# Optimization experiments

Hardware: AMD Instinct MI355X
Metric: run time of the kernel (lower is better)

Reference implementation:

```python
import jax, jax.numpy as jnp
from jax import lax
import numpy as np

NBC, NAC, KF, RHO = 14, 45, 52, 0.05
KT = np.arange(0.8, 0, -1.0 / 64, dtype=np.float32)[None, :]  # (1, 52) AC kernel time axis
K = KT.shape[1]


def _sigm(x, off, slope):
    return jax.nn.sigmoid(slope * (x - off))


def _ac_kernel(log_tr, log_td, kt):
    tr = jnp.exp(log_tr)[:, None]  # (nAC,1)
    td = jnp.exp(log_td)[:, None]
    k = jnp.exp(-kt / td) - jnp.exp(-(td + tr) / (td * tr) * kt)  # (nAC,K)
    return k / jnp.linalg.norm(k, axis=1, keepdims=True)


def setup_inputs() -> dict:
    key = jax.random.key(0)
    ks = jax.random.split(key, 12)
    B, T = 64, 4096
    n = 0.01  # noise_init_scale
    return {
        "x": jax.random.normal(ks[0], (B, T), jnp.float32) * 0.5,
        "bc_kernels": jax.random.normal(ks[1], (NBC, KF), jnp.float32) * 0.1,
        "log_sigmoid_slope": jnp.log(2.0) + n * jax.random.normal(ks[2], (NBC,), jnp.float32),
        "sigmoid_offset": 1.5 + n * jax.random.normal(ks[3], (NBC,), jnp.float32),
        "log_bc_ac_weight": jnp.log(1.0 / NBC) + n * jax.random.normal(ks[4], (NAC, NBC), jnp.float32),
        "log_ac_tau_rise": jnp.log(0.1) + n * jax.random.normal(ks[5], (NAC,), jnp.float32),
        "log_ac_tau_decay": jnp.log(0.1) + n * jax.random.normal(ks[6], (NAC,), jnp.float32),
        "log_ac_sigmoid_slope": jnp.log(2.0) + n * jax.random.normal(ks[7], (NAC,), jnp.float32),
        "ac_sigmoid_offset": 1.5 + n * jax.random.normal(ks[8], (NAC,), jnp.float32),
        "log_ac_bc_weight": jnp.log(0.01) + n * jax.random.normal(ks[9], (NBC, NAC), jnp.float32),
        "out_scale": jnp.ones((NBC,), jnp.float32),
    }


def reference(x, bc_kernels, log_sigmoid_slope, sigmoid_offset, log_bc_ac_weight,
              log_ac_tau_rise, log_ac_tau_decay, log_ac_sigmoid_slope,
              ac_sigmoid_offset, log_ac_bc_weight, out_scale):
    B, T = x.shape
    kt = jnp.asarray(KT)
    # linear_filter: causal conv of stimulus with per-BC kernels -> (T, B, nBC)
    xf = lax.conv_general_dilated(x[:, None, :], bc_kernels[:, None, :], (1,), [(KF - 1, 0)])
    xf = jnp.transpose(xf, (2, 0, 1))  # (T, B, nBC)

    slope = jnp.exp(log_sigmoid_slope)
    ac_slope = jnp.exp(log_ac_sigmoid_slope)
    bc_ac_w = jnp.exp(log_bc_ac_weight)          # (nAC, nBC)
    ac_bc_w = -jnp.exp(log_ac_bc_weight)         # (nBC, nAC)
    ack = _ac_kernel(log_ac_tau_rise, log_ac_tau_decay, kt)  # (nAC, K)

    # --- plain LNR branch (no feedback) ---
    prob_lnr = _sigm(xf, sigmoid_offset, slope)

    def lnr_step(pool, p):
        pool2 = pool + (1.0 - pool) * RHO
        rel = p * pool2
        return pool2 - rel, rel

    _, rel_lnr = lax.scan(lnr_step, jnp.ones((B, NBC), x.dtype), prob_lnr)
    y_lnr = (out_scale * rel_lnr).transpose(1, 0, 2)  # (B, T, nBC)

    # --- BCN branch with AC feedback recurrence ---
    def bcn_step(carry, xt):
        pool, prev_rel, buf = carry
        # append previous release (track_release[i-1]) to sliding window (oldest first)
        buf = jnp.concatenate([buf[..., 1:], prev_rel[..., None]], axis=-1)  # (B, nBC, K)
        drive = jnp.einsum('ak,ab,nbk->na', ack, bc_ac_w, buf)               # (B, nAC)
        ac_out = _sigm(drive, ac_sigmoid_offset, ac_slope)
        fb = ac_out @ ac_bc_w.T                                              # (B, nBC)
        prob = _sigm(xt + fb, sigmoid_offset, slope)
        pool2 = pool + (1.0 - pool) * RHO
        rel = prob * pool2
        return (pool2 - rel, rel, buf), (rel, fb, ac_out)

    init = (jnp.ones((B, NBC), x.dtype), jnp.zeros((B, NBC), x.dtype), jnp.zeros((B, NBC, K), x.dtype))
    _, (rel, fb, ac_out) = lax.scan(bcn_step, init, xf)
    y_bcn = (out_scale * rel).transpose(1, 0, 2)  # (B, T, nBC)
    return y_bcn, fb.transpose(1, 0, 2), ac_out.transpose(1, 0, 2), y_lnr
```

## Files before the change

### kernel.cpp

```cpp
#include <hip/hip_runtime.h>
#include <hip/hip_fp16.h>

#define NBC 14
#define NAC 45
#define KF  52
#define RHO 0.05f
#define TT  4096
#define BB  64
#define CHC 64
#define WU  44
#define NPAIR 32
#define NTW (WU + CHC)
#define SPAN (WU + 2*CHC)
#define XPAD 176
#define LOG2E 1.44269504f
#define XF_BYTES ((size_t)BB * NBC * TT * 2)

typedef __fp16 v2h __attribute__((ext_vector_type(2)));
typedef float  f2  __attribute__((ext_vector_type(2)));
typedef int    i2v __attribute__((ext_vector_type(2)));

__device__ __forceinline__ v2h bch(unsigned u) { return __builtin_bit_cast(v2h, u); }
__device__ __forceinline__ unsigned bcu(v2h h) { return __builtin_bit_cast(unsigned, h); }
__device__ __forceinline__ v2h pk2(float lo, float hi) {
#if __has_builtin(__builtin_amdgcn_cvt_pkrtz)
  return __builtin_bit_cast(v2h, __builtin_amdgcn_cvt_pkrtz(lo, hi));
#else
  v2h r; r[0] = (__fp16)lo; r[1] = (__fp16)hi; return r;
#endif
}
__device__ __forceinline__ v2h xsum16h(v2h v) {
#if __has_builtin(__builtin_amdgcn_permlane16_swap)
  i2v r = __builtin_amdgcn_permlane16_swap((int)bcu(v), (int)bcu(v), false, false);
  return bch((unsigned)r[0]) + bch((unsigned)r[1]);
#else
  return v + bch((unsigned)__builtin_amdgcn_ds_swizzle((int)bcu(v), (16 << 10) | 0x1f));
#endif
}
__device__ __forceinline__ v2h xsum32h(v2h v) {
#if __has_builtin(__builtin_amdgcn_permlane32_swap)
  i2v r = __builtin_amdgcn_permlane32_swap((int)bcu(v), (int)bcu(v), false, false);
  return bch((unsigned)r[0]) + bch((unsigned)r[1]);
#else
  return v + bch((unsigned)__shfl_xor((int)bcu(v), 32));
#endif
}
__device__ __forceinline__ float exp2_f(float x) {
#if __has_builtin(__builtin_amdgcn_exp2f)
  return __builtin_amdgcn_exp2f(x);
#else
  return exp2f(x);
#endif
}

__global__ __launch_bounds__(256)
void conv_kernel(const float* __restrict__ x, const float* __restrict__ bck,
                 __half* __restrict__ xfg) {
  __shared__ float xs[256 + KF];
  const int tid  = threadIdx.x;
  const int b    = blockIdx.x >> 4;
  const int t0   = (blockIdx.x & 15) << 8;
  for (int i = tid; i < 256 + KF - 1; i += 256) {
    int gt = t0 - (KF - 1) + i;
    xs[i] = (gt >= 0) ? x[b * TT + gt] : 0.f;
  }
  __syncthreads();
  float acc[NBC];
#pragma unroll
  for (int c = 0; c < NBC; ++c) acc[c] = 0.f;
#pragma unroll 4
  for (int k = 0; k < KF; ++k) {
    float xv = xs[tid + k];
#pragma unroll
    for (int c = 0; c < NBC; ++c) acc[c] = fmaf(bck[c * KF + k], xv, acc[c]);
  }
#pragma unroll
  for (int c = 0; c < NBC; ++c)
    xfg[((size_t)b * NBC + c) * TT + t0 + tid] = __float2half(acc[c]);
}

#define POOL_BYTES 6144

template<bool PRECONV>
__global__ __launch_bounds__(64)
void bcn_kernel(const float* __restrict__ x,
                const float* __restrict__ bck,
                const float* __restrict__ lss,
                const float* __restrict__ soff,
                const float* __restrict__ lbaw,
                const float* __restrict__ ltr,
                const float* __restrict__ ltd,
                const float* __restrict__ lass,
                const float* __restrict__ asoff,
                const float* __restrict__ labw,
                const float* __restrict__ oscale,
                const __half* __restrict__ xfg,
                float* __restrict__ out)
{
  __shared__ __align__(16) char pool[POOL_BYTES];
  __half*   xf_lds = (__half*)pool;
  unsigned* acr    = (unsigned*)(pool + 4928);
  unsigned* relr   = (unsigned*)(pool + 5184);
  float*    x_lds  = (float*)(pool + 5248);

  const int lid   = threadIdx.x;
  const int c16   = lid & 15;
  const int q     = lid >> 4;
  const float rowm = (q & 1) ? 0.f : 1.f;
  const int blk   = blockIdx.x;
  const int b     = blk >> 5;
  const int p     = blk & 31;
  const int t0A   = p * (2 * CHC);
  const int t_begin = t0A - WU;

  if constexpr (PRECONV) {
    const __half* src = xfg + (size_t)b * NBC * TT;
    if (p == 0) {
      for (int e = lid; e < NBC * SPAN; e += 64) {
        int c = e / SPAN, i = e - c * SPAN;
        int gt = t_begin + i; if (gt < 0) gt = 0;
        xf_lds[c * XPAD + i] = src[(size_t)c * TT + gt];
      }
    } else {
      for (int c = 0; c < NBC; ++c) {
        if (lid < SPAN / 4) {
          uint2 v = *(const uint2*)(src + (size_t)c * TT + t_begin + 4 * lid);
          *(uint2*)&xf_lds[c * XPAD + 4 * lid] = v;
        }
      }
    }
  } else {
    for (int i = lid; i < SPAN + KF - 1; i += 64) {
      int gt = t_begin - (KF - 1) + i;
      x_lds[i] = (gt >= 0) ? x[b * TT + gt] : 0.f;
    }
    __syncthreads();
    for (int ib = 0; ib < 3; ++ib) {
      int tau = lid + (ib << 6);
      if (tau < SPAN) {
        float acc[NBC];
#pragma unroll
        for (int c = 0; c < NBC; ++c) acc[c] = 0.f;
#pragma unroll 4
        for (int k = 0; k < KF; ++k) {
          float xv = x_lds[tau + k];
#pragma unroll
          for (int c = 0; c < NBC; ++c) acc[c] = fmaf(bck[c * KF + k], xv, acc[c]);
        }
#pragma unroll
        for (int c = 0; c < NBC; ++c) xf_lds[c * XPAD + tau] = __float2half(acc[c]);
      }
    }
    __syncthreads();
  }

  if (lid < 64) acr[lid] = 0u;
  if (lid < 16) relr[lid] = 0u;

  float slope2 = 0.f, soff2 = 0.f, osc_c = 0.f;
  f2 poolP; poolP.x = 1.f; poolP.y = 1.f;
  f2 SA; SA.x = 0.f; SA.y = 0.f;
  f2 SB; SB.x = 0.f; SB.y = 0.f;
  f2 rv2, cn2; rv2.x = rv2.y = cn2.x = cn2.y = 0.f;
  float Adrv2 = 0.f, Boff2 = 0.f;
  v2h wfbh[16];
  v2h wuh[NBC];
  f2 yst[4], fst[4];
  unsigned acst[4];

#pragma unroll
  for (int j = 0; j < 16; ++j) wfbh[j] = pk2(0.f, 0.f);
#pragma unroll
  for (int c = 0; c < NBC; ++c) wuh[c] = pk2(0.f, 0.f);

  if (c16 < NBC) {
    float sl = expf(lss[c16]);
    slope2 = sl * LOG2E;
    soff2  = soff[c16] * sl * LOG2E;
    osc_c  = oscale[c16];
#pragma unroll
    for (int j = 0; j < 16; ++j) {
      int a = 16 * q + j;
      if (a < NAC) { float w = -expf(labw[c16 * NAC + a]); wfbh[j] = pk2(w, w); }
    }
  }
  if (lid < NAC) {
    float tr = expf(ltr[lid]);
    float td = expf(ltd[lid]);
    float a1 = 1.f / td;
    float gg = (td + tr) / (td * tr);
    rv2.x = expf(-a1 * 0.015625f);  rv2.y = expf(-gg * 0.015625f);
    cn2.x = expf(-a1 * 0.003125f);  cn2.y = expf(-gg * 0.003125f);
    float nrm = 0.f;
    for (int k = 0; k < KF; ++k) {
      float kt = 0.8f - (float)k * 0.015625f;
      float d = expf(-a1 * kt) - expf(-gg * kt);
      nrm = fmaf(d, d, nrm);
    }
    float inorm  = 1.f / sqrtf(nrm);
    float aslope = expf(lass[lid]);
    Adrv2 = aslope * inorm * LOG2E;
    Boff2 = aslope * asoff[lid] * LOG2E;
#pragma unroll
    for (int c = 0; c < NBC; ++c) {
      float w = expf(lbaw[lid * NBC + c]);
      wuh[c] = pk2(w, w);
    }
  }

  float* yb  = out;
  float* fbp = out + (size_t)BB * TT * NBC;
  float* acp = out + 2 * (size_t)BB * TT * NBC;
  float* ylp = out + 2 * (size_t)BB * TT * NBC + (size_t)BB * TT * NAC;

  __syncthreads();

  auto step = [&](int slot4, float xfA, float xfB, bool emit)
      __attribute__((always_inline)) {
    float mzA = fmaf(-Adrv2, SA.x - SA.y, Boff2);
    float mzB = fmaf(-Adrv2, SB.x - SB.y, Boff2);
    float acA = __fdividef(1.f, 1.f + exp2_f(mzA));
    float acB = __fdividef(1.f, 1.f + exp2_f(mzB));
    if (lid < NAC) acr[lid] = bcu(pk2(acA, acB));

    const uint4* ab = (const uint4*)(acr + (q << 4));
    uint4 A0 = ab[0], A1 = ab[1], A2 = ab[2], A3 = ab[3];
    v2h g0 = wfbh[0] * bch(A0.x);
    v2h g1 = wfbh[1] * bch(A0.y);
    g0 += wfbh[2]  * bch(A0.z);  g1 += wfbh[3]  * bch(A0.w);
    g0 += wfbh[4]  * bch(A1.x);  g1 += wfbh[5]  * bch(A1.y);
    g0 += wfbh[6]  * bch(A1.z);  g1 += wfbh[7]  * bch(A1.w);
    g0 += wfbh[8]  * bch(A2.x);  g1 += wfbh[9]  * bch(A2.y);
    g0 += wfbh[10] * bch(A2.z);  g1 += wfbh[11] * bch(A2.w);
    g0 += wfbh[12] * bch(A3.x);  g1 += wfbh[13] * bch(A3.y);
    g0 += wfbh[14] * bch(A3.z);  g1 += wfbh[15] * bch(A3.w);
    v2h gs = xsum32h(xsum16h(g0 + g1));
    float fbA = (float)gs[0], fbB = (float)gs[1];

    float mA = fmaf(-slope2, fmaf(rowm, fbA, xfA), soff2);
    float mB = fmaf(-slope2, fmaf(rowm, fbB, xfB), soff2);
    f2 pv;
    pv.x = __fdividef(1.f, 1.f + exp2_f(mA));
    pv.y = __fdividef(1.f, 1.f + exp2_f(mB));
    f2 p2 = poolP * (1.f - RHO) + RHO;
    f2 relP = pv * p2;
    poolP = p2 - relP;
    if (lid < NBC) relr[lid] = bcu(pk2(relP.x, relP.y));
    if (emit) {
      yst[slot4] = relP * osc_c;
      f2 t; t.x = fbA; t.y = fbB; fst[slot4] = t;
      acst[slot4] = bcu(pk2(acA, acB));
    }

    const uint4* rb = (const uint4*)relr;
    uint4 R0 = rb[0], R1 = rb[1], R2 = rb[2], R3 = rb[3];
    v2h h0 = wuh[0] * bch(R0.x);
    v2h h1 = wuh[1] * bch(R0.y);
    h0 += wuh[2]  * bch(R0.z);  h1 += wuh[3]  * bch(R0.w);
    h0 += wuh[4]  * bch(R1.x);  h1 += wuh[5]  * bch(R1.y);
    h0 += wuh[6]  * bch(R1.z);  h1 += wuh[7]  * bch(R1.w);
    h0 += wuh[8]  * bch(R2.x);  h1 += wuh[9]  * bch(R2.y);
    h0 += wuh[10] * bch(R2.z);  h1 += wuh[11] * bch(R2.w);
    h0 += wuh[12] * bch(R3.x);  h1 += wuh[13] * bch(R3.y);
    v2h uh = h0 + h1;
    SA = SA * rv2 + cn2 * (float)uh[0];
    SB = SB * rv2 + cn2 * (float)uh[1];
  };

  auto group = [&](int s4, bool emit) __attribute__((always_inline)) {
    uint2 xa = *(const uint2*)&xf_lds[c16 * XPAD + s4];
    uint2 xb = *(const uint2*)&xf_lds[c16 * XPAD + s4 + CHC];
    v2h xA01 = bch(xa.x), xA23 = bch(xa.y);
    v2h xB01 = bch(xb.x), xB23 = bch(xb.y);
    step(0, (float)xA01[0], (float)xB01[0], emit);
    step(1, (float)xA01[1], (float)xB01[1], emit);
    step(2, (float)xA23[0], (float)xB23[0], emit);
    step(3, (float)xA23[1], (float)xB23[1], emit);
  };

  for (int s4 = 0; s4 < WU; s4 += 4) group(s4, false);

  if (p == 0) {
    SA.x = 0.f; SA.y = 0.f;
    poolP.x = 1.f;
  }

  for (int s4 = WU; s4 < NTW; s4 += 4) {
    group(s4, true);

    int tgA = t0A + (s4 - WU);
    size_t baseA = (size_t)b * TT + tgA;
    if (lid < NBC) {
      size_t ob = baseA * NBC + lid;
#pragma unroll
      for (int sl = 0; sl < 4; ++sl) {
        yb [ob + sl * NBC]                     = yst[sl].x;
        yb [ob + (size_t)CHC * NBC + sl * NBC] = yst[sl].y;
        fbp[ob + sl * NBC]                     = fst[sl].x;
        fbp[ob + (size_t)CHC * NBC + sl * NBC] = fst[sl].y;
      }
    } else if (lid >= 16 && lid < 16 + NBC) {
      size_t ob = baseA * NBC + (lid - 16);
#pragma unroll
      for (int sl = 0; sl < 4; ++sl) {
        ylp[ob + sl * NBC]                     = yst[sl].x;
        ylp[ob + (size_t)CHC * NBC + sl * NBC] = yst[sl].y;
      }
    }
    if (lid < NAC) {
      size_t oa = baseA * NAC + lid;
#pragma unroll
      for (int sl = 0; sl < 4; ++sl) {
        v2h h = bch(acst[sl]);
        acp[oa + sl * NAC]                     = (float)h[0];
        acp[oa + (size_t)CHC * NAC + sl * NAC] = (float)h[1];
      }
    }
  }
}

extern "C" void kernel_launch(void* const* d_in, const int* in_sizes, int n_in,
                              void* d_out, int out_size, void* d_ws, size_t ws_size,
                              hipStream_t stream) {
  (void)in_sizes; (void)n_in; (void)out_size;
  const float* x    = (const float*)d_in[0];
  const float* bck  = (const float*)d_in[1];
  if (ws_size >= XF_BYTES) {
    __half* xfg = (__half*)d_ws;
    conv_kernel<<<dim3(BB * 16), dim3(256), 0, stream>>>(x, bck, xfg);
    bcn_kernel<true><<<dim3(BB * NPAIR), dim3(64), 0, stream>>>(
        x, bck, (const float*)d_in[2], (const float*)d_in[3], (const float*)d_in[4],
        (const float*)d_in[5], (const float*)d_in[6], (const float*)d_in[7],
        (const float*)d_in[8], (const float*)d_in[9], (const float*)d_in[10],
        xfg, (float*)d_out);
  } else {
    bcn_kernel<false><<<dim3(BB * NPAIR), dim3(64), 0, stream>>>(
        x, bck, (const float*)d_in[2], (const float*)d_in[3], (const float*)d_in[4],
        (const float*)d_in[5], (const float*)d_in[6], (const float*)d_in[7],
        (const float*)d_in[8], (const float*)d_in[9], (const float*)d_in[10],
        (const __half*)nullptr, (float*)d_out);
  }
}
```

Measured before the change: 91.35 us.

## Process four time chunks per wavefront instead of two in BCN recurrence

```diff
diff --git a/kernel.cpp b/kernel.cpp
--- a/kernel.cpp
+++ b/kernel.cpp
@@ -9,10 +9,10 @@
 #define BB  64
 #define CHC 64
 #define WU  44
-#define NPAIR 32
+#define NQUAD 16
 #define NTW (WU + CHC)
-#define SPAN (WU + 2*CHC)
-#define XPAD 176
+#define SPAN (WU + 4*CHC)
+#define XPAD 304
 #define LOG2E 1.44269504f
 #define XF_BYTES ((size_t)BB * NBC * TT * 2)
 
@@ -79,7 +79,7 @@
     xfg[((size_t)b * NBC + c) * TT + t0 + tid] = __float2half(acc[c]);
 }
 
-#define POOL_BYTES 6144
+#define POOL_BYTES 10560
 
 template<bool PRECONV>
 __global__ __launch_bounds__(64)
@@ -99,18 +99,20 @@
 {
   __shared__ __align__(16) char pool[POOL_BYTES];
   __half*   xf_lds = (__half*)pool;
-  unsigned* acr    = (unsigned*)(pool + 4928);
-  unsigned* relr   = (unsigned*)(pool + 5184);
-  float*    x_lds  = (float*)(pool + 5248);
+  unsigned* acr1   = (unsigned*)(pool + 8512);
+  unsigned* acr2   = (unsigned*)(pool + 8768);
+  unsigned* relr1  = (unsigned*)(pool + 9024);
+  unsigned* relr2  = (unsigned*)(pool + 9088);
+  float*    x_lds  = (float*)(pool + 9152);
 
   const int lid   = threadIdx.x;
   const int c16   = lid & 15;
   const int q     = lid >> 4;
   const float rowm = (q & 1) ? 0.f : 1.f;
   const int blk   = blockIdx.x;
-  const int b     = blk >> 5;
-  const int p     = blk & 31;
-  const int t0A   = p * (2 * CHC);
+  const int b     = blk >> 4;
+  const int p     = blk & 15;
+  const int t0A   = p * (4 * CHC);
   const int t_begin = t0A - WU;
 
   if constexpr (PRECONV) {
@@ -122,11 +124,10 @@
         xf_lds[c * XPAD + i] = src[(size_t)c * TT + gt];
       }
     } else {
-      for (int c = 0; c < NBC; ++c) {
-        if (lid < SPAN / 4) {
-          uint2 v = *(const uint2*)(src + (size_t)c * TT + t_begin + 4 * lid);
-          *(uint2*)&xf_lds[c * XPAD + 4 * lid] = v;
-        }
+      for (int e = lid; e < NBC * (SPAN / 4); e += 64) {
+        int c = e / (SPAN / 4), i = e - c * (SPAN / 4);
+        uint2 v = *(const uint2*)(src + (size_t)c * TT + t_begin + 4 * i);
+        *(uint2*)&xf_lds[c * XPAD + 4 * i] = v;
       }
     }
   } else {
@@ -135,7 +136,7 @@
       x_lds[i] = (gt >= 0) ? x[b * TT + gt] : 0.f;
     }
     __syncthreads();
-    for (int ib = 0; ib < 3; ++ib) {
+    for (int ib = 0; ib < 5; ++ib) {
       int tau = lid + (ib << 6);
       if (tau < SPAN) {
         float acc[NBC];
@@ -154,19 +155,22 @@
     __syncthreads();
   }
 
-  if (lid < 64) acr[lid] = 0u;
-  if (lid < 16) relr[lid] = 0u;
+  if (lid < 64) { acr1[lid] = 0u; acr2[lid] = 0u; }
+  if (lid < 16) { relr1[lid] = 0u; relr2[lid] = 0u; }
 
   float slope2 = 0.f, soff2 = 0.f, osc_c = 0.f;
-  f2 poolP; poolP.x = 1.f; poolP.y = 1.f;
+  f2 poolP1; poolP1.x = 1.f; poolP1.y = 1.f;
+  f2 poolP2; poolP2.x = 1.f; poolP2.y = 1.f;
   f2 SA; SA.x = 0.f; SA.y = 0.f;
   f2 SB; SB.x = 0.f; SB.y = 0.f;
+  f2 SC; SC.x = 0.f; SC.y = 0.f;
+  f2 SD; SD.x = 0.f; SD.y = 0.f;
   f2 rv2, cn2; rv2.x = rv2.y = cn2.x = cn2.y = 0.f;
   float Adrv2 = 0.f, Boff2 = 0.f;
   v2h wfbh[16];
   v2h wuh[NBC];
-  f2 yst[4], fst[4];
-  unsigned acst[4];
+  f2 yst1[4], fst1[4], yst2[4], fst2[4];
+  unsigned acst1[4], acst2[4];
 
 #pragma unroll
   for (int j = 0; j < 16; ++j) wfbh[j] = pk2(0.f, 0.f);
@@ -215,105 +219,151 @@
 
   __syncthreads();
 
-  auto step = [&](int slot4, float xfA, float xfB, bool emit)
+  auto step = [&](int slot4, float xA, float xB, float xC, float xD, bool emit)
       __attribute__((always_inline)) {
     float mzA = fmaf(-Adrv2, SA.x - SA.y, Boff2);
     float mzB = fmaf(-Adrv2, SB.x - SB.y, Boff2);
+    float mzC = fmaf(-Adrv2, SC.x - SC.y, Boff2);
+    float mzD = fmaf(-Adrv2, SD.x - SD.y, Boff2);
     float acA = __fdividef(1.f, 1.f + exp2_f(mzA));
     float acB = __fdividef(1.f, 1.f + exp2_f(mzB));
-    if (lid < NAC) acr[lid] = bcu(pk2(acA, acB));
-
-    const uint4* ab = (const uint4*)(acr + (q << 4));
-    uint4 A0 = ab[0], A1 = ab[1], A2 = ab[2], A3 = ab[3];
-    v2h g0 = wfbh[0] * bch(A0.x);
-    v2h g1 = wfbh[1] * bch(A0.y);
-    g0 += wfbh[2]  * bch(A0.z);  g1 += wfbh[3]  * bch(A0.w);
-    g0 += wfbh[4]  * bch(A1.x);  g1 += wfbh[5]  * bch(A1.y);
-    g0 += wfbh[6]  * bch(A1.z);  g1 += wfbh[7]  * bch(A1.w);
-    g0 += wfbh[8]  * bch(A2.x);  g1 += wfbh[9]  * bch(A2.y);
-    g0 += wfbh[10] * bch(A2.z);  g1 += wfbh[11] * bch(A2.w);
-    g0 += wfbh[12] * bch(A3.x);  g1 += wfbh[13] * bch(A3.y);
-    g0 += wfbh[14] * bch(A3.z);  g1 += wfbh[15] * bch(A3.w);
-    v2h gs = xsum32h(xsum16h(g0 + g1));
-    float fbA = (float)gs[0], fbB = (float)gs[1];
-
-    float mA = fmaf(-slope2, fmaf(rowm, fbA, xfA), soff2);
-    float mB = fmaf(-slope2, fmaf(rowm, fbB, xfB), soff2);
-    f2 pv;
-    pv.x = __fdividef(1.f, 1.f + exp2_f(mA));
-    pv.y = __fdividef(1.f, 1.f + exp2_f(mB));
-    f2 p2 = poolP * (1.f - RHO) + RHO;
-    f2 relP = pv * p2;
-    poolP = p2 - relP;
-    if (lid < NBC) relr[lid] = bcu(pk2(relP.x, relP.y));
+    float acC = __fdividef(1.f, 1.f + exp2_f(mzC));
+    float acD = __fdividef(1.f, 1.f + exp2_f(mzD));
+    if (lid < NAC) { acr1[lid] = bcu(pk2(acA, acB)); acr2[lid] = bcu(pk2(acC, acD)); }
+
+    const uint4* ab1 = (const uint4*)(acr1 + (q << 4));
+    const uint4* ab2 = (const uint4*)(acr2 + (q << 4));
+    uint4 P0 = ab1[0], P1 = ab1[1], P2 = ab1[2], P3 = ab1[3];
+    uint4 Q0 = ab2[0], Q1 = ab2[1], Q2 = ab2[2], Q3 = ab2[3];
+    v2h g0 = wfbh[0] * bch(P0.x), g1 = wfbh[1] * bch(P0.y);
+    v2h e0 = wfbh[0] * bch(Q0.x), e1 = wfbh[1] * bch(Q0.y);
+    g0 += wfbh[2]  * bch(P0.z);  g1 += wfbh[3]  * bch(P0.w);
+    e0 += wfbh[2]  * bch(Q0.z);  e1 += wfbh[3]  * bch(Q0.w);
+    g0 += wfbh[4]  * bch(P1.x);  g1 += wfbh[5]  * bch(P1.y);
+    e0 += wfbh[4]  * bch(Q1.x);  e1 += wfbh[5]  * bch(Q1.y);
+    g0 += wfbh[6]  * bch(P1.z);  g1 += wfbh[7]  * bch(P1.w);
+    e0 += wfbh[6]  * bch(Q1.z);  e1 += wfbh[7]  * bch(Q1.w);
+    g0 += wfbh[8]  * bch(P2.x);  g1 += wfbh[9]  * bch(P2.y);
+    e0 += wfbh[8]  * bch(Q2.x);  e1 += wfbh[9]  * bch(Q2.y);
+    g0 += wfbh[10] * bch(P2.z);  g1 += wfbh[11] * bch(P2.w);
+    e0 += wfbh[10] * bch(Q2.z);  e1 += wfbh[11] * bch(Q2.w);
+    g0 += wfbh[12] * bch(P3.x);  g1 += wfbh[13] * bch(P3.y);
+    e0 += wfbh[12] * bch(Q3.x);  e1 += wfbh[13] * bch(Q3.y);
+    g0 += wfbh[14] * bch(P3.z);  g1 += wfbh[15] * bch(P3.w);
+    e0 += wfbh[14] * bch(Q3.z);  e1 += wfbh[15] * bch(Q3.w);
+    v2h gs1 = xsum32h(xsum16h(g0 + g1));
+    v2h gs2 = xsum32h(xsum16h(e0 + e1));
+    float fbA = (float)gs1[0], fbB = (float)gs1[1];
+    float fbC = (float)gs2[0], fbD = (float)gs2[1];
+
+    float mA = fmaf(-slope2, fmaf(rowm, fbA, xA), soff2);
+    float mB = fmaf(-slope2, fmaf(rowm, fbB, xB), soff2);
+    float mC = fmaf(-slope2, fmaf(rowm, fbC, xC), soff2);
+    float mD = fmaf(-slope2, fmaf(rowm, fbD, xD), soff2);
+    f2 pv1, pv2;
+    pv1.x = __fdividef(1.f, 1.f + exp2_f(mA));
+    pv1.y = __fdividef(1.f, 1.f + exp2_f(mB));
+    pv2.x = __fdividef(1.f, 1.f + exp2_f(mC));
+    pv2.y = __fdividef(1.f, 1.f + exp2_f(mD));
+    f2 p21 = poolP1 * (1.f - RHO) + RHO;
+    f2 p22 = poolP2 * (1.f - RHO) + RHO;
+    f2 rel1 = pv1 * p21, rel2 = pv2 * p22;
+    poolP1 = p21 - rel1;  poolP2 = p22 - rel2;
+    if (lid < NBC) { relr1[lid] = bcu(pk2(rel1.x, rel1.y));
+                     relr2[lid] = bcu(pk2(rel2.x, rel2.y)); }
     if (emit) {
-      yst[slot4] = relP * osc_c;
-      f2 t; t.x = fbA; t.y = fbB; fst[slot4] = t;
-      acst[slot4] = bcu(pk2(acA, acB));
-    }
-
-    const uint4* rb = (const uint4*)relr;
-    uint4 R0 = rb[0], R1 = rb[1], R2 = rb[2], R3 = rb[3];
-    v2h h0 = wuh[0] * bch(R0.x);
-    v2h h1 = wuh[1] * bch(R0.y);
+      yst1[slot4] = rel1 * osc_c;  yst2[slot4] = rel2 * osc_c;
+      f2 t1; t1.x = fbA; t1.y = fbB; fst1[slot4] = t1;
+      f2 t2; t2.x = fbC; t2.y = fbD; fst2[slot4] = t2;
+      acst1[slot4] = bcu(pk2(acA, acB));
+      acst2[slot4] = bcu(pk2(acC, acD));
+    }
+
+    const uint4* rb1 = (const uint4*)relr1;
+    const uint4* rb2 = (const uint4*)relr2;
+    uint4 R0 = rb1[0], R1 = rb1[1], R2 = rb1[2], R3 = rb1[3];
+    uint4 T0 = rb2[0], T1 = rb2[1], T2 = rb2[2], T3 = rb2[3];
+    v2h h0 = wuh[0] * bch(R0.x), h1 = wuh[1] * bch(R0.y);
+    v2h k0 = wuh[0] * bch(T0.x), k1 = wuh[1] * bch(T0.y);
     h0 += wuh[2]  * bch(R0.z);  h1 += wuh[3]  * bch(R0.w);
+    k0 += wuh[2]  * bch(T0.z);  k1 += wuh[3]  * bch(T0.w);
     h0 += wuh[4]  * bch(R1.x);  h1 += wuh[5]  * bch(R1.y);
+    k0 += wuh[4]  * bch(T1.x);  k1 += wuh[5]  * bch(T1.y);
     h0 += wuh[6]  * bch(R1.z);  h1 += wuh[7]  * bch(R1.w);
+    k0 += wuh[6]  * bch(T1.z);  k1 += wuh[7]  * bch(T1.w);
     h0 += wuh[8]  * bch(R2.x);  h1 += wuh[9]  * bch(R2.y);
+    k0 += wuh[8]  * bch(T2.x);  k1 += wuh[9]  * bch(T2.y);
     h0 += wuh[10] * bch(R2.z);  h1 += wuh[11] * bch(R2.w);
+    k0 += wuh[10] * bch(T2.z);  k1 += wuh[11] * bch(T2.w);
     h0 += wuh[12] * bch(R3.x);  h1 += wuh[13] * bch(R3.y);
-    v2h uh = h0 + h1;
-    SA = SA * rv2 + cn2 * (float)uh[0];
-    SB = SB * rv2 + cn2 * (float)uh[1];
+    k0 += wuh[12] * bch(T3.x);  k1 += wuh[13] * bch(T3.y);
+    v2h uh1 = h0 + h1, uh2 = k0 + k1;
+    SA = SA * rv2 + cn2 * (float)uh1[0];
+    SB = SB * rv2 + cn2 * (float)uh1[1];
+    SC = SC * rv2 + cn2 * (float)uh2[0];
+    SD = SD * rv2 + cn2 * (float)uh2[1];
   };
 
   auto group = [&](int s4, bool emit) __attribute__((always_inline)) {
     uint2 xa = *(const uint2*)&xf_lds[c16 * XPAD + s4];
     uint2 xb = *(const uint2*)&xf_lds[c16 * XPAD + s4 + CHC];
-    v2h xA01 = bch(xa.x), xA23 = bch(xa.y);
-    v2h xB01 = bch(xb.x), xB23 = bch(xb.y);
-    step(0, (float)xA01[0], (float)xB01[0], emit);
-    step(1, (float)xA01[1], (float)xB01[1], emit);
-    step(2, (float)xA23[0], (float)xB23[0], emit);
-    step(3, (float)xA23[1], (float)xB23[1], emit);
+    uint2 xc = *(const uint2*)&xf_lds[c16 * XPAD + s4 + 2 * CHC];
+    uint2 xd = *(const uint2*)&xf_lds[c16 * XPAD + s4 + 3 * CHC];
+    v2h a01 = bch(xa.x), a23 = bch(xa.y);
+    v2h b01 = bch(xb.x), b23 = bch(xb.y);
+    v2h c01 = bch(xc.x), c23 = bch(xc.y);
+    v2h d01 = bch(xd.x), d23 = bch(xd.y);
+    step(0, (float)a01[0], (float)b01[0], (float)c01[0], (float)d01[0], emit);
+    step(1, (float)a01[1], (float)b01[1], (float)c01[1], (float)d01[1], emit);
+    step(2, (float)a23[0], (float)b23[0], (float)c23[0], (float)d23[0], emit);
+    step(3, (float)a23[1], (float)b23[1], (float)c23[1], (float)d23[1], emit);
   };
 
   for (int s4 = 0; s4 < WU; s4 += 4) group(s4, false);
 
   if (p == 0) {
     SA.x = 0.f; SA.y = 0.f;
-    poolP.x = 1.f;
+    poolP1.x = 1.f;
   }
 
   for (int s4 = WU; s4 < NTW; s4 += 4) {
     group(s4, true);
 
-    int tgA = t0A + (s4 - WU);
-    size_t baseA = (size_t)b * TT + tgA;
+    int tg = t0A + (s4 - WU);
+    size_t base = (size_t)b * TT + tg;
     if (lid < NBC) {
-      size_t ob = baseA * NBC + lid;
+      size_t ob = base * NBC + lid;
 #pragma unroll
       for (int sl = 0; sl < 4; ++sl) {
-        yb [ob + sl * NBC]                     = yst[sl].x;
-        yb [ob + (size_t)CHC * NBC + sl * NBC] = yst[sl].y;
-        fbp[ob + sl * NBC]                     = fst[sl].x;
-        fbp[ob + (size_t)CHC * NBC + sl * NBC] = fst[sl].y;
+        yb [ob + sl * NBC]                         = yst1[sl].x;
+        yb [ob + (size_t)CHC * NBC + sl * NBC]     = yst1[sl].y;
+        yb [ob + 2 * (size_t)CHC * NBC + sl * NBC] = yst2[sl].x;
+        yb [ob + 3 * (size_t)CHC * NBC + sl * NBC] = yst2[sl].y;
+        fbp[ob + sl * NBC]                         = fst1[sl].x;
+        fbp[ob + (size_t)CHC * NBC + sl * NBC]     = fst1[sl].y;
+        fbp[ob + 2 * (size_t)CHC * NBC + sl * NBC] = fst2[sl].x;
+        fbp[ob + 3 * (size_t)CHC * NBC + sl * NBC] = fst2[sl].y;
       }
     } else if (lid >= 16 && lid < 16 + NBC) {
-      size_t ob = baseA * NBC + (lid - 16);
+      size_t ob = base * NBC + (lid - 16);
 #pragma unroll
       for (int sl = 0; sl < 4; ++sl) {
-        ylp[ob + sl * NBC]                     = yst[sl].x;
-        ylp[ob + (size_t)CHC * NBC + sl * NBC] = yst[sl].y;
+        ylp[ob + sl * NBC]                         = yst1[sl].x;
+        ylp[ob + (size_t)CHC * NBC + sl * NBC]     = yst1[sl].y;
+        ylp[ob + 2 * (size_t)CHC * NBC + sl * NBC] = yst2[sl].x;
+        ylp[ob + 3 * (size_t)CHC * NBC + sl * NBC] = yst2[sl].y;
       }
     }
     if (lid < NAC) {
-      size_t oa = baseA * NAC + lid;
+      size_t oa = base * NAC + lid;
 #pragma unroll
       for (int sl = 0; sl < 4; ++sl) {
-        v2h h = bch(acst[sl]);
-        acp[oa + sl * NAC]                     = (float)h[0];
-        acp[oa + (size_t)CHC * NAC + sl * NAC] = (float)h[1];
+        v2h h1 = bch(acst1[sl]);
+        v2h h2 = bch(acst2[sl]);
+        acp[oa + sl * NAC]                         = (float)h1[0];
+        acp[oa + (size_t)CHC * NAC + sl * NAC]     = (float)h1[1];
+        acp[oa + 2 * (size_t)CHC * NAC + sl * NAC] = (float)h2[0];
+        acp[oa + 3 * (size_t)CHC * NAC + sl * NAC] = (float)h2[1];
       }
     }
   }
@@ -328,13 +378,13 @@
   if (ws_size >= XF_BYTES) {
     __half* xfg = (__half*)d_ws;
     conv_kernel<<<dim3(BB * 16), dim3(256), 0, stream>>>(x, bck, xfg);
-    bcn_kernel<true><<<dim3(BB * NPAIR), dim3(64), 0, stream>>>(
+    bcn_kernel<true><<<dim3(BB * NQUAD), dim3(64), 0, stream>>>(
         x, bck, (const float*)d_in[2], (const float*)d_in[3], (const float*)d_in[4],
         (const float*)d_in[5], (const float*)d_in[6], (const float*)d_in[7],
         (const float*)d_in[8], (const float*)d_in[9], (const float*)d_in[10],
         xfg, (float*)d_out);
   } else {
-    bcn_kernel<false><<<dim3(BB * NPAIR), dim3(64), 0, stream>>>(
+    bcn_kernel<false><<<dim3(BB * NQUAD), dim3(64), 0, stream>>>(
         x, bck, (const float*)d_in[2], (const float*)d_in[3], (const float*)d_in[4],
         (const float*)d_in[5], (const float*)d_in[6], (const float*)d_in[7],
         (const float*)d_in[8], (const float*)d_in[9], (const float*)d_in[10],
```

New measurement: 100.4 us. 1.1x slower.
